# Kernel tuning notes

Hardware: AMD Instinct MI355X
Metric: run time of the kernel (lower is better)

The kernel has to match this reference:

```python
import jax, jax.numpy as jnp
import numpy as np

K = 7          # kernel_size
PAD = 3        # padding
EPS = 1e-8


def setup_inputs() -> dict:
    key = jax.random.key(0)
    x = jax.random.normal(key, (32, 3, 512, 512), dtype=jnp.float32)
    return {"x": x}


def reference(x) -> jnp.ndarray:
    # Faithful fused version of: unfold -> center/neighbor cosine distance -> sum/8.
    # stride=1, dilation=1, padding=3, kernel=7 => output spatial size == input size,
    # and the patch center (flat index 24) is exactly the unpadded pixel itself.
    B, C, H, W = x.shape
    xp = jnp.pad(x, ((0, 0), (0, 0), (PAD, PAD), (PAD, PAD)))
    center = x  # == xp[:, :, PAD:PAD+H, PAD:PAD+W]
    # ||center|| over channels, clamped (matches .norm(dim=1).clamp_min(eps))
    cn = jnp.maximum(jnp.sqrt(jnp.sum(center * center, axis=1)), EPS)  # (B,H,W)
    acc = jnp.zeros((B, H, W), dtype=x.dtype)
    mid = K // 2
    for i in range(K):  # small fixed 7x7 loop; avoids materializing (B,C,49,H*W)
        for j in range(K):
            if i == mid and j == mid:
                continue  # skip center (neighbor_idx excludes center_flat)
            nb = xp[:, :, i:i + H, j:j + W]                      # (B,C,H,W)
            dot = jnp.sum(center * nb, axis=1)                   # (B,H,W)
            nn_ = jnp.maximum(jnp.sqrt(jnp.sum(nb * nb, axis=1)), EPS)
            acc = acc + (1.0 - dot / (cn * nn_))
    out = acc / 8.0  # module hardcodes /8 despite 48 neighbors
    return out[:, None, :, :]  # (B,1,H,W)
```

## Files before the change

### kernel.cpp

```cpp
#include <hip/hip_runtime.h>


typedef unsigned int u32;
typedef float f32x4 __attribute__((ext_vector_type(4)));

#define EPS2 1e-16f

constexpr int HR = 15;

__device__ __forceinline__ u32 packbf2(float a, float b) {
    const u32 ua = __float_as_uint(a), ub = __float_as_uint(b);
    return ((ua + 0x8000u) >> 16) | ((ub + 0x8000u) & 0xffff0000u);
}
__device__ __forceinline__ float uplo(u32 u) { return __uint_as_float(u << 16); }
__device__ __forceinline__ float uphi(u32 u) { return __uint_as_float(u & 0xffff0000u); }
__device__ __forceinline__ f32x4 vmul(f32x4 v, float s) {
    f32x4 r; r[0]=v[0]*s; r[1]=v[1]*s; r[2]=v[2]*s; r[3]=v[3]*s; return r;
}

__global__ __launch_bounds__(256, 4) void mcnd_kernel(const float* __restrict__ x,
                                                      float* __restrict__ out,
                                                      int B, int H, int W) {
    __shared__ uint4 hsh[4][3][8][HR];

    const int HW = H * W;
    const int tilesX = W >> 6;
    const int tilesPerImg = tilesX * (H >> 5);

    const int cpx  = gridDim.x >> 3;
    const int wgid = (blockIdx.x & 7) * cpx + (blockIdx.x >> 3);
    const int b    = wgid / tilesPerImg;
    const int t    = wgid % tilesPerImg;
    const int ty   = t / tilesX;
    const int tx   = t - ty * tilesX;
    const int x0   = tx << 6;

    const int wv   = threadIdx.x >> 6;
    const int lane = threadIdx.x & 63;
    const int r    = lane >> 3;
    const int grp  = lane & 7;
    const int yw   = (ty << 5) + (wv << 3);

    const float* __restrict__ xb = x + (size_t)b * 3 * HW;

    const int   gxl   = x0 + (grp << 3) - 4;
    const float lmask = (gxl >= 0) ? 1.f : 0.f;
    const float rmask = (gxl + 16 <= W) ? 1.f : 0.f;
    const int   gofL  = (gxl >= 0) ? gxl : 0;
    const int   gofR  = (gxl + 16 <= W) ? (gxl + 12) : (W - 4);

    u32 gc0[4], gc1[4], gc2[4];

    auto process = [&](int hr, bool capture) {
        const int   gy  = yw + hr - 3;
        const float rmk = (gy >= 0 && gy < H) ? 1.f : 0.f;
        const int   gyc = gy < 0 ? 0 : (gy >= H ? H - 1 : gy);
        const float* rp0 = xb + (size_t)gyc * W;
        const float* rp1 = rp0 + HW;
        const float* rp2 = rp1 + HW;
        f32x4 a0 = *(const f32x4*)(rp0 + gofL);
        f32x4 a1 = *(const f32x4*)(rp0 + gxl + 4);
        f32x4 a2 = *(const f32x4*)(rp0 + gxl + 8);
        f32x4 a3 = *(const f32x4*)(rp0 + gofR);
        f32x4 b0 = *(const f32x4*)(rp1 + gofL);
        f32x4 b1 = *(const f32x4*)(rp1 + gxl + 4);
        f32x4 b2 = *(const f32x4*)(rp1 + gxl + 8);
        f32x4 b3 = *(const f32x4*)(rp1 + gofR);
        f32x4 c0 = *(const f32x4*)(rp2 + gofL);
        f32x4 c1 = *(const f32x4*)(rp2 + gxl + 4);
        f32x4 c2 = *(const f32x4*)(rp2 + gxl + 8);
        f32x4 c3 = *(const f32x4*)(rp2 + gofR);
        a0 = vmul(a0, lmask); b0 = vmul(b0, lmask); c0 = vmul(c0, lmask);
        a3 = vmul(a3, rmask); b3 = vmul(b3, rmask); c3 = vmul(c3, rmask);
        f32x4 i0, i1, i2, i3;
        {
            const f32x4 n0 = a0*a0 + b0*b0 + c0*c0;
            const f32x4 n1 = a1*a1 + b1*b1 + c1*c1;
            const f32x4 n2 = a2*a2 + b2*b2 + c2*c2;
            const f32x4 n3 = a3*a3 + b3*b3 + c3*c3;
#pragma unroll
            for (int e = 0; e < 4; ++e) {
                i0[e] = __builtin_amdgcn_rsqf(fmaxf(n0[e], EPS2)) * rmk;
                i1[e] = __builtin_amdgcn_rsqf(fmaxf(n1[e], EPS2)) * rmk;
                i2[e] = __builtin_amdgcn_rsqf(fmaxf(n2[e], EPS2)) * rmk;
                i3[e] = __builtin_amdgcn_rsqf(fmaxf(n3[e], EPS2)) * rmk;
            }
        }
        auto chan = [&](const f32x4& A0, const f32x4& A1, const f32x4& A2,
                        const f32x4& A3, int ch, u32* gcp) {
            float cc[16];
#pragma unroll
            for (int e = 0; e < 4; ++e) {
                cc[e]      = A0[e] * i0[e];
                cc[4 + e]  = A1[e] * i1[e];
                cc[8 + e]  = A2[e] * i2[e];
                cc[12 + e] = A3[e] * i3[e];
            }
            float hp[8];
            hp[0] = cc[1]+cc[2]+cc[3]+cc[4]+cc[5]+cc[6]+cc[7];
#pragma unroll
            for (int m = 1; m < 8; ++m) hp[m] = hp[m-1] - cc[m] + cc[m+7];
            uint4 hwv;
            hwv.x = packbf2(hp[0], hp[1]); hwv.y = packbf2(hp[2], hp[3]);
            hwv.z = packbf2(hp[4], hp[5]); hwv.w = packbf2(hp[6], hp[7]);
            hsh[wv][ch][grp][hr] = hwv;
            if (capture) {
                gcp[0] = packbf2(cc[4],  cc[5]);
                gcp[1] = packbf2(cc[6],  cc[7]);
                gcp[2] = packbf2(cc[8],  cc[9]);
                gcp[3] = packbf2(cc[10], cc[11]);
            }
        };
        chan(a0, a1, a2, a3, 0, gc0);
        chan(b0, b1, b2, b3, 1, gc1);
        chan(c0, c1, c2, c3, 2, gc2);
    };

    process(r + 3, true);
    if (lane < 48) {
        const int rr = lane >> 3;
        process(rr < 3 ? rr : rr + 8, false);
    }
    asm volatile("s_waitcnt lgkmcnt(0)" ::: "memory");
    __builtin_amdgcn_sched_barrier(0);

    float D[8] = {0.f,0.f,0.f,0.f,0.f,0.f,0.f,0.f};
    auto vch = [&](int ch, const u32* gcp) {
        float s[8] = {0.f,0.f,0.f,0.f,0.f,0.f,0.f,0.f};
#pragma unroll
        for (int d = 0; d < 7; ++d) {
            const uint4 u = hsh[wv][ch][grp][r + d];
            s[0] += uplo(u.x); s[1] += uphi(u.x);
            s[2] += uplo(u.y); s[3] += uphi(u.y);
            s[4] += uplo(u.z); s[5] += uphi(u.z);
            s[6] += uplo(u.w); s[7] += uphi(u.w);
        }
#pragma unroll
        for (int e = 0; e < 8; ++e) {
            const u32 gu = gcp[e >> 1];
            const float gv = (e & 1) ? uphi(gu) : uplo(gu);
            D[e] += gv * s[e];
        }
    };
    vch(0, gc0); vch(1, gc1); vch(2, gc2);

    f32x4 o0, o1;
#pragma unroll
    for (int e = 0; e < 8; ++e) {
        const float v = (49.0f - D[e]) * 0.125f;
        if (e < 4) o0[e] = v; else o1[e - 4] = v;
    }
    float* op = out + (size_t)b * HW + (size_t)(yw + r) * W + (x0 + (grp << 3));
    *(f32x4*)(op)     = o0;
    *(f32x4*)(op + 4) = o1;
}

extern "C" void kernel_launch(void* const* d_in, const int* in_sizes, int n_in,
                              void* d_out, int out_size, void* d_ws, size_t ws_size,
                              hipStream_t stream) {
    (void)n_in; (void)d_ws; (void)ws_size; (void)out_size;
    const float* x = (const float*)d_in[0];
    float* out = (float*)d_out;

    const int H = 512, W = 512, C = 3;
    const int B = in_sizes[0] / (C * H * W);

    const int tilesPerImg = (W >> 6) * (H >> 5);
    mcnd_kernel<<<B * tilesPerImg, 256, 0, stream>>>(x, out, B, H, W);
}
```

Before: 36.32 us.

## Compute two output rows per thread with sliding vertical box sum

Each wave now covers 16 rows instead of 8 and each thread produces two adjacent output rows. The second row's vertical 7-row sum is derived from the first by subtracting the top row and adding a new bottom row. This cuts the halo rows loaded and processed per output (6 halo rows per 16 instead of per 8) and reduces shared-memory reads per output. In exchange there are half as many blocks, more registers per thread, and a larger shared buffer, which may lower occupancy.

```diff
diff --git a/kernel.cpp b/kernel.cpp
--- a/kernel.cpp
+++ b/kernel.cpp
@@ -6,7 +6,7 @@
 
 #define EPS2 1e-16f
 
-constexpr int HR = 15;
+constexpr int HRS = 23;
 
 __device__ __forceinline__ u32 packbf2(float a, float b) {
     const u32 ua = __float_as_uint(a), ub = __float_as_uint(b);
@@ -21,11 +21,11 @@
 __global__ __launch_bounds__(256, 4) void mcnd_kernel(const float* __restrict__ x,
                                                       float* __restrict__ out,
                                                       int B, int H, int W) {
-    __shared__ uint4 hsh[4][3][8][HR];
+    __shared__ uint4 hsh[4][3][8][HRS];
 
     const int HW = H * W;
     const int tilesX = W >> 6;
-    const int tilesPerImg = tilesX * (H >> 5);
+    const int tilesPerImg = tilesX * (H >> 6);
 
     const int cpx  = gridDim.x >> 3;
     const int wgid = (blockIdx.x & 7) * cpx + (blockIdx.x >> 3);
@@ -37,9 +37,9 @@
 
     const int wv   = threadIdx.x >> 6;
     const int lane = threadIdx.x & 63;
-    const int r    = lane >> 3;
+    const int r2   = lane >> 3;
     const int grp  = lane & 7;
-    const int yw   = (ty << 5) + (wv << 3);
+    const int yw   = (ty << 6) + (wv << 4);
 
     const float* __restrict__ xb = x + (size_t)b * 3 * HW;
 
@@ -49,9 +49,10 @@
     const int   gofL  = (gxl >= 0) ? gxl : 0;
     const int   gofR  = (gxl + 16 <= W) ? (gxl + 12) : (W - 4);
 
-    u32 gc0[4], gc1[4], gc2[4];
+    u32 gA0[4], gA1[4], gA2[4];
+    u32 gB0[4], gB1[4], gB2[4];
 
-    auto process = [&](int hr, bool capture) {
+    auto process = [&](int hr, u32* cp0, u32* cp1, u32* cp2) {
         const int   gy  = yw + hr - 3;
         const float rmk = (gy >= 0 && gy < H) ? 1.f : 0.f;
         const int   gyc = gy < 0 ? 0 : (gy >= H ? H - 1 : gy);
@@ -104,55 +105,76 @@
             hwv.x = packbf2(hp[0], hp[1]); hwv.y = packbf2(hp[2], hp[3]);
             hwv.z = packbf2(hp[4], hp[5]); hwv.w = packbf2(hp[6], hp[7]);
             hsh[wv][ch][grp][hr] = hwv;
-            if (capture) {
+            if (gcp) {
                 gcp[0] = packbf2(cc[4],  cc[5]);
                 gcp[1] = packbf2(cc[6],  cc[7]);
                 gcp[2] = packbf2(cc[8],  cc[9]);
                 gcp[3] = packbf2(cc[10], cc[11]);
             }
         };
-        chan(a0, a1, a2, a3, 0, gc0);
-        chan(b0, b1, b2, b3, 1, gc1);
-        chan(c0, c1, c2, c3, 2, gc2);
+        chan(a0, a1, a2, a3, 0, cp0);
+        chan(b0, b1, b2, b3, 1, cp1);
+        chan(c0, c1, c2, c3, 2, cp2);
     };
 
-    process(r + 3, true);
+    process(2*r2 + 3, gA0, gA1, gA2);
+    process(2*r2 + 4, gB0, gB1, gB2);
     if (lane < 48) {
         const int rr = lane >> 3;
-        process(rr < 3 ? rr : rr + 8, false);
+        process(rr < 3 ? rr : rr + 16, nullptr, nullptr, nullptr);
     }
     asm volatile("s_waitcnt lgkmcnt(0)" ::: "memory");
     __builtin_amdgcn_sched_barrier(0);
 
-    float D[8] = {0.f,0.f,0.f,0.f,0.f,0.f,0.f,0.f};
-    auto vch = [&](int ch, const u32* gcp) {
-        float s[8] = {0.f,0.f,0.f,0.f,0.f,0.f,0.f,0.f};
+    float D0[8] = {0.f,0.f,0.f,0.f,0.f,0.f,0.f,0.f};
+    float D1[8] = {0.f,0.f,0.f,0.f,0.f,0.f,0.f,0.f};
+    auto vch = [&](int ch, const u32* ga, const u32* gb) {
+        float acc[8] = {0.f,0.f,0.f,0.f,0.f,0.f,0.f,0.f};
+        float f0[8], f7[8];
 #pragma unroll
-        for (int d = 0; d < 7; ++d) {
-            const uint4 u = hsh[wv][ch][grp][r + d];
-            s[0] += uplo(u.x); s[1] += uphi(u.x);
-            s[2] += uplo(u.y); s[3] += uphi(u.y);
-            s[4] += uplo(u.z); s[5] += uphi(u.z);
-            s[6] += uplo(u.w); s[7] += uphi(u.w);
+        for (int d = 0; d < 8; ++d) {
+            const uint4 u = hsh[wv][ch][grp][2*r2 + d];
+            float a[8];
+            a[0] = uplo(u.x); a[1] = uphi(u.x);
+            a[2] = uplo(u.y); a[3] = uphi(u.y);
+            a[4] = uplo(u.z); a[5] = uphi(u.z);
+            a[6] = uplo(u.w); a[7] = uphi(u.w);
+            if (d == 0) {
+#pragma unroll
+                for (int e = 0; e < 8; ++e) f0[e] = a[e];
+            }
+            if (d == 7) {
+#pragma unroll
+                for (int e = 0; e < 8; ++e) f7[e] = a[e];
+            } else {
+#pragma unroll
+                for (int e = 0; e < 8; ++e) acc[e] += a[e];
+            }
         }
 #pragma unroll
         for (int e = 0; e < 8; ++e) {
-            const u32 gu = gcp[e >> 1];
-            const float gv = (e & 1) ? uphi(gu) : uplo(gu);
-            D[e] += gv * s[e];
+            const u32 gau = ga[e >> 1], gbu = gb[e >> 1];
+            const float gav = (e & 1) ? uphi(gau) : uplo(gau);
+            const float gbv = (e & 1) ? uphi(gbu) : uplo(gbu);
+            D0[e] += gav * acc[e];
+            D1[e] += gbv * (acc[e] - f0[e] + f7[e]);
         }
     };
-    vch(0, gc0); vch(1, gc1); vch(2, gc2);
+    vch(0, gA0, gB0); vch(1, gA1, gB1); vch(2, gA2, gB2);
 
-    f32x4 o0, o1;
+    f32x4 o00, o01, o10, o11;
 #pragma unroll
     for (int e = 0; e < 8; ++e) {
-        const float v = (49.0f - D[e]) * 0.125f;
-        if (e < 4) o0[e] = v; else o1[e - 4] = v;
+        const float v0 = (49.0f - D0[e]) * 0.125f;
+        const float v1 = (49.0f - D1[e]) * 0.125f;
+        if (e < 4) { o00[e] = v0; o10[e] = v1; }
+        else       { o01[e - 4] = v0; o11[e - 4] = v1; }
     }
-    float* op = out + (size_t)b * HW + (size_t)(yw + r) * W + (x0 + (grp << 3));
-    *(f32x4*)(op)     = o0;
-    *(f32x4*)(op + 4) = o1;
+    float* op = out + (size_t)b * HW + (size_t)(yw + 2*r2) * W + (x0 + (grp << 3));
+    *(f32x4*)(op)         = o00;
+    *(f32x4*)(op + 4)     = o01;
+    *(f32x4*)(op + W)     = o10;
+    *(f32x4*)(op + W + 4) = o11;
 }
 
 extern "C" void kernel_launch(void* const* d_in, const int* in_sizes, int n_in,
@@ -165,6 +187,6 @@
     const int H = 512, W = 512, C = 3;
     const int B = in_sizes[0] / (C * H * W);
 
-    const int tilesPerImg = (W >> 6) * (H >> 5);
+    const int tilesPerImg = (W >> 6) * (H >> 6);
     mcnd_kernel<<<B * tilesPerImg, 256, 0, stream>>>(x, out, B, H, W);
 }
```

Result: slower. 48.50 us (+33.5%).
